# Kernel optimization log

Hardware: AMD Instinct MI355X
Metric: run time of the kernel (lower is better)

The kernel has to match this reference:

```python
import jax, jax.numpy as jnp
import numpy as np

QLEN, MLEN, BSZ, DMODEL, NHEAD, DHEAD = 512, 512, 8, 1024, 16, 64
KLEN = QLEN + MLEN
LN_EPS = 1e-5


def layer_norm(x, g, b):
    mu = jnp.mean(x, axis=-1, keepdims=True)
    var = jnp.var(x, axis=-1, keepdims=True)
    return (x - mu) / jnp.sqrt(var + LN_EPS) * g + b


def rel_shift(x):
    # x: [qlen, klen, bsz, n_head] -- Transformer-XL relative shift trick
    q, k, b, n = x.shape
    x_pad = jnp.pad(x, ((0, 0), (1, 0), (0, 0), (0, 0)))  # zero col at front of dim 1
    x_pad = x_pad.reshape(k + 1, q, b, n)
    return x_pad[1:].reshape(q, k, b, n)


def setup_inputs() -> dict:
    key = jax.random.key(0)
    ks = jax.random.split(key, 10)
    w = lambda k, shape: (jax.random.normal(k, shape, jnp.float32) * 0.02)
    return {
        "content": jax.random.normal(ks[0], (QLEN, BSZ, DMODEL), jnp.float32),
        "mems": jax.random.normal(ks[1], (MLEN, BSZ, DMODEL), jnp.float32),
        "r": jax.random.normal(ks[2], (KLEN, DMODEL), jnp.float32),
        "q_bias": w(ks[3], (NHEAD, DHEAD)),
        "mask": jnp.zeros((QLEN, KLEN, BSZ), jnp.bool_),
        "W_q": w(ks[4], (NHEAD * DHEAD, DMODEL)),
        "W_kv": w(ks[5], (2 * NHEAD * DHEAD, DMODEL)),
        "W_r": w(ks[6], (NHEAD * DHEAD, DMODEL)),
        "b_r": jnp.zeros((NHEAD * DHEAD,), jnp.float32),
        "W_o": w(ks[7], (DMODEL, NHEAD * DHEAD)),
        "b_o": jnp.zeros((DMODEL,), jnp.float32),
        "ln_g": jnp.ones((DMODEL,), jnp.float32),
        "ln_b": jnp.zeros((DMODEL,), jnp.float32),
    }


def reference(content, mems, r, q_bias, mask, W_q, W_kv, W_r, b_r, W_o, b_o, ln_g, ln_b):
    Q, B, D = content.shape
    H, Dh = q_bias.shape
    scale = 1.0 / (Dh ** 0.5)

    c = layer_norm(content, ln_g, ln_b)          # [Q,B,D]
    m = layer_norm(mems, ln_g, ln_b)             # [M,B,D]
    cat = jnp.concatenate([m, c], axis=0)        # [K,B,D]
    K = cat.shape[0]

    kv = cat @ W_kv.T                            # [K,B,2*H*Dh]
    k, v = jnp.split(kv, 2, axis=-1)
    k = k.reshape(K, B, H, Dh)
    v = v.reshape(K, B, H, Dh)

    q = (c @ W_q.T).reshape(Q, B, H, Dh) + q_bias  # [Q,B,H,Dh]
    rproj = (r @ W_r.T + b_r).reshape(K, H, Dh)    # [K,H,Dh]

    AC = jnp.einsum('ibnd,jbnd->ijbn', q, k)       # content-content
    BD = rel_shift(jnp.einsum('ibnd,jnd->ijbn', q, rproj))  # content-position
    score = (AC + BD) * scale                      # [Q,K,B,H]
    score = jnp.where(mask[..., None], -jnp.inf, score)
    prob = jax.nn.softmax(score, axis=1)

    vec = jnp.einsum('ijbn,jbnd->ibnd', prob, v).reshape(Q, B, H * Dh)
    attn_out = vec @ W_o.T + b_o                   # [Q,B,D]
    # IdentityResidualGate: x + relu(y) with x = layer-normed content
    return c + jax.nn.relu(attn_out)
```

## Files before the change

kernel.cpp:

```cpp
#include <hip/hip_runtime.h>
#include <hip/hip_bf16.h>
#include <math.h>

#define QLEN 512
#define MLENC 512
#define KLEN 1024
#define BSZ 8
#define DMODEL 1024
#define NHEAD 16
#define DHEAD 64

typedef __hip_bfloat16 bf16;
typedef unsigned short u16;
typedef unsigned int u32;
typedef __attribute__((ext_vector_type(8))) short s16x8;
typedef __attribute__((ext_vector_type(4))) float f32x4;

#define MFMA16(a, b, c) __builtin_amdgcn_mfma_f32_16x16x32_bf16(a, b, c, 0, 0, 0)

static __device__ __forceinline__ float b2f(bf16 x) { return __bfloat162float(x); }
static __device__ __forceinline__ bf16 f2b(float x) { return __float2bfloat16(x); }
static __device__ __forceinline__ u16 bbu(float x) {
    bf16 h = __float2bfloat16(x);
    return *reinterpret_cast<u16*>(&h);
}
static __device__ __forceinline__ u32 pk2(float a, float b) {
    return ((u32)bbu(b) << 16) | bbu(a);
}

static __device__ __forceinline__ void gl_lds16(const void* g, void* l) {
    __builtin_amdgcn_global_load_lds(
        (const __attribute__((address_space(1))) void*)g,
        (__attribute__((address_space(3))) void*)l, 16, 0, 0);
}

template <int MODE, bool AF32, bool BF32>
static __device__ __forceinline__ void gemm128_dev(const void* __restrict__ Av,
                                                   const void* __restrict__ Bv,
                                                   const float* __restrict__ bias,
                                                   const bf16* __restrict__ resid,
                                                   bf16* __restrict__ Cb,
                                                   float* __restrict__ Cf,
                                                   int m0, int n0, int N,
                                                   short* As, short* Bs) {
    int tid = threadIdx.x;
    int w = tid >> 6, lane = tid & 63, l15 = lane & 15, quad = lane >> 4;
    int wm = w & 1, wn = w >> 1;

    const short* Ab = (const short*)Av;
    const float* Af = (const float*)Av;
    const short* Bb = (const short*)Bv;
    const float* Bf = (const float*)Bv;

    f32x4 acc[4][4];
#pragma unroll
    for (int i = 0; i < 4; ++i)
#pragma unroll
        for (int j = 0; j < 4; ++j) acc[i][j] = (f32x4){0.f, 0.f, 0.f, 0.f};

    for (int kt = 0; kt < 1024; kt += 64) {
        __syncthreads();
        if (!AF32) {
#pragma unroll
            for (int li = 0; li < 4; ++li) {
                int id = (li * 4 + w) * 64 + lane;
                int row = id >> 3;
                int kc = ((id & 7) ^ (row & 7)) * 8;
                gl_lds16(Ab + ((size_t)(m0 + row) * 1024 + kt + kc),
                         &As[(li * 4 + w) * 512]);
            }
        } else {
            int m = tid >> 1, kcl = (tid & 1) * 32;
            const float* src = Af + (size_t)(m0 + m) * 1024 + kt + kcl;
#pragma unroll
            for (int ch = 0; ch < 4; ++ch) {
                int cl = (kcl >> 3) + ch;
                u32* dst = (u32*)&As[m * 64 + ((cl ^ (m & 7)) * 8)];
                float4 f0 = *(const float4*)(src + ch * 8);
                float4 f1 = *(const float4*)(src + ch * 8 + 4);
                dst[0] = pk2(f0.x, f0.y); dst[1] = pk2(f0.z, f0.w);
                dst[2] = pk2(f1.x, f1.y); dst[3] = pk2(f1.z, f1.w);
            }
        }
        if (!BF32) {
#pragma unroll
            for (int li = 0; li < 4; ++li) {
                int id = (li * 4 + w) * 64 + lane;
                int row = id >> 3;
                int kc = ((id & 7) ^ (row & 7)) * 8;
                gl_lds16(Bb + ((size_t)(n0 + row) * 1024 + kt + kc),
                         &Bs[(li * 4 + w) * 512]);
            }
        } else {
            int nn = tid >> 1, kcl = (tid & 1) * 32;
            const float* src = Bf + (size_t)(n0 + nn) * 1024 + kt + kcl;
#pragma unroll
            for (int ch = 0; ch < 4; ++ch) {
                int cl = (kcl >> 3) + ch;
                u32* dst = (u32*)&Bs[nn * 64 + ((cl ^ (nn & 7)) * 8)];
                float4 f0 = *(const float4*)(src + ch * 8);
                float4 f1 = *(const float4*)(src + ch * 8 + 4);
                dst[0] = pk2(f0.x, f0.y); dst[1] = pk2(f0.z, f0.w);
                dst[2] = pk2(f1.x, f1.y); dst[3] = pk2(f1.z, f1.w);
            }
        }
        __syncthreads();

        s16x8 af[4][2], bfr[4][2];
#pragma unroll
        for (int mb = 0; mb < 4; ++mb) {
            int row = wm * 64 + mb * 16 + l15;
#pragma unroll
            for (int kh = 0; kh < 2; ++kh)
                af[mb][kh] = *(const s16x8*)
                    &As[row * 64 + (((kh * 4 + quad) ^ (row & 7)) * 8)];
        }
#pragma unroll
        for (int nb = 0; nb < 4; ++nb) {
            int row = wn * 64 + nb * 16 + l15;
#pragma unroll
            for (int kh = 0; kh < 2; ++kh)
                bfr[nb][kh] = *(const s16x8*)
                    &Bs[row * 64 + (((kh * 4 + quad) ^ (row & 7)) * 8)];
        }
#pragma unroll
        for (int mb = 0; mb < 4; ++mb)
#pragma unroll
            for (int nb = 0; nb < 4; ++nb) {
                acc[mb][nb] = MFMA16(af[mb][0], bfr[nb][0], acc[mb][nb]);
                acc[mb][nb] = MFMA16(af[mb][1], bfr[nb][1], acc[mb][nb]);
            }
    }

#pragma unroll
    for (int mb = 0; mb < 4; ++mb) {
#pragma unroll
        for (int nb = 0; nb < 4; ++nb) {
#pragma unroll
            for (int r = 0; r < 4; ++r) {
                int m = m0 + wm * 64 + mb * 16 + quad * 4 + r;
                int col = n0 + wn * 64 + nb * 16 + l15;
                float v = acc[mb][nb][r];
                if (MODE >= 1) v += bias[col];
                if (MODE == 2) {
                    float rv = b2f(resid[(size_t)m * N + col]);
                    Cf[(size_t)m * N + col] = rv + fmaxf(v, 0.f);
                } else {
                    Cb[(size_t)m * N + col] = f2b(v);
                }
            }
        }
    }
}

template <int MODE, bool AF32, bool BF32>
static __device__ __forceinline__ void gemm64_dev(const void* __restrict__ Av,
                                                  const void* __restrict__ Bv,
                                                  const float* __restrict__ bias,
                                                  const bf16* __restrict__ resid,
                                                  bf16* __restrict__ Cb,
                                                  float* __restrict__ Cf,
                                                  int m0, int n0, int N,
                                                  short* As, short* Bs) {
    int tid = threadIdx.x;
    int w = tid >> 6, lane = tid & 63, l15 = lane & 15, quad = lane >> 4;

    const short* Ab = (const short*)Av;
    const float* Af = (const float*)Av;
    const short* Bb = (const short*)Bv;
    const float* Bf = (const float*)Bv;

    f32x4 acc[4][2];
#pragma unroll
    for (int i = 0; i < 4; ++i)
#pragma unroll
        for (int j = 0; j < 2; ++j) acc[i][j] = (f32x4){0.f, 0.f, 0.f, 0.f};

    for (int kt = 0; kt < 1024; kt += 64) {
        __syncthreads();
        if (!AF32) {
#pragma unroll
            for (int li = 0; li < 2; ++li) {
                int id = (li * 4 + w) * 64 + lane;
                int row = id >> 3;
                int kc = ((id & 7) ^ (row & 7)) * 8;
                gl_lds16(Ab + ((size_t)(m0 + row) * 1024 + kt + kc),
                         &As[(li * 4 + w) * 512]);
            }
        } else {
            int m = tid >> 2, kcl = (tid & 3) * 16;
            const float* src = Af + (size_t)(m0 + m) * 1024 + kt + kcl;
#pragma unroll
            for (int ch = 0; ch < 2; ++ch) {
                int cl = (kcl >> 3) + ch;
                u32* dst = (u32*)&As[m * 64 + ((cl ^ (m & 7)) * 8)];
                float4 f0 = *(const float4*)(src + ch * 8);
                float4 f1 = *(const float4*)(src + ch * 8 + 4);
                dst[0] = pk2(f0.x, f0.y); dst[1] = pk2(f0.z, f0.w);
                dst[2] = pk2(f1.x, f1.y); dst[3] = pk2(f1.z, f1.w);
            }
        }
        if (!BF32) {
#pragma unroll
            for (int li = 0; li < 4; ++li) {
                int id = (li * 4 + w) * 64 + lane;
                int row = id >> 3;
                int kc = ((id & 7) ^ (row & 7)) * 8;
                gl_lds16(Bb + ((size_t)(n0 + row) * 1024 + kt + kc),
                         &Bs[(li * 4 + w) * 512]);
            }
        } else {
            int nn = tid >> 1, kcl = (tid & 1) * 32;
            const float* src = Bf + (size_t)(n0 + nn) * 1024 + kt + kcl;
#pragma unroll
            for (int ch = 0; ch < 4; ++ch) {
                int cl = (kcl >> 3) + ch;
                u32* dst = (u32*)&Bs[nn * 64 + ((cl ^ (nn & 7)) * 8)];
                float4 f0 = *(const float4*)(src + ch * 8);
                float4 f1 = *(const float4*)(src + ch * 8 + 4);
                dst[0] = pk2(f0.x, f0.y); dst[1] = pk2(f0.z, f0.w);
                dst[2] = pk2(f1.x, f1.y); dst[3] = pk2(f1.z, f1.w);
            }
        }
        __syncthreads();

        s16x8 af[4][2], bfr[2][2];
#pragma unroll
        for (int mb = 0; mb < 4; ++mb) {
            int row = mb * 16 + l15;
#pragma unroll
            for (int kh = 0; kh < 2; ++kh)
                af[mb][kh] = *(const s16x8*)
                    &As[row * 64 + (((kh * 4 + quad) ^ (row & 7)) * 8)];
        }
#pragma unroll
        for (int nb = 0; nb < 2; ++nb) {
            int row = w * 32 + nb * 16 + l15;
#pragma unroll
            for (int kh = 0; kh < 2; ++kh)
                bfr[nb][kh] = *(const s16x8*)
                    &Bs[row * 64 + (((kh * 4 + quad) ^ (row & 7)) * 8)];
        }
#pragma unroll
        for (int mb = 0; mb < 4; ++mb)
#pragma unroll
            for (int nb = 0; nb < 2; ++nb) {
                acc[mb][nb] = MFMA16(af[mb][0], bfr[nb][0], acc[mb][nb]);
                acc[mb][nb] = MFMA16(af[mb][1], bfr[nb][1], acc[mb][nb]);
            }
    }

#pragma unroll
    for (int mb = 0; mb < 4; ++mb) {
#pragma unroll
        for (int nb = 0; nb < 2; ++nb) {
#pragma unroll
            for (int r = 0; r < 4; ++r) {
                int m = m0 + mb * 16 + quad * 4 + r;
                int col = n0 + w * 32 + nb * 16 + l15;
                float v = acc[mb][nb][r];
                if (MODE >= 1) v += bias[col];
                if (MODE == 2) {
                    float rv = b2f(resid[(size_t)m * N + col]);
                    Cf[(size_t)m * N + col] = rv + fmaxf(v, 0.f);
                } else {
                    Cb[(size_t)m * N + col] = f2b(v);
                }
            }
        }
    }
}

static __device__ __forceinline__ void ln_body(int row, int tid,
                                               const float* __restrict__ content,
                                               const float* __restrict__ mems,
                                               const float* __restrict__ g,
                                               const float* __restrict__ bet,
                                               bf16* __restrict__ cat,
                                               float* red) {
    const float* src = (row < MLENC * BSZ)
        ? mems + (size_t)row * DMODEL
        : content + (size_t)(row - MLENC * BSZ) * DMODEL;

    float x[4];
    float s = 0.f, ss = 0.f;
#pragma unroll
    for (int l = 0; l < 4; ++l) {
        int d = l * 256 + tid;
        x[l] = src[d];
        s += x[l];
        ss += x[l] * x[l];
    }
#pragma unroll
    for (int off = 32; off > 0; off >>= 1) {
        s  += __shfl_xor(s, off);
        ss += __shfl_xor(ss, off);
    }
    int wid = tid >> 6;
    if ((tid & 63) == 0) { red[wid * 2] = s; red[wid * 2 + 1] = ss; }
    __syncthreads();
    s  = red[0] + red[2] + red[4] + red[6];
    ss = red[1] + red[3] + red[5] + red[7];
    float mu  = s * (1.f / DMODEL);
    float var = ss * (1.f / DMODEL) - mu * mu;
    float rs  = rsqrtf(var + 1e-5f);
    bf16* dst = cat + (size_t)row * DMODEL;
#pragma unroll
    for (int l = 0; l < 4; ++l) {
        int d = l * 256 + tid;
        dst[d] = f2b((x[l] - mu) * rs * g[d] + bet[d]);
    }
}

__global__ __launch_bounds__(256) void ln_kernel(const float* __restrict__ content,
                                                 const float* __restrict__ mems,
                                                 const float* __restrict__ g,
                                                 const float* __restrict__ bet,
                                                 bf16* __restrict__ cat) {
    __shared__ float red[8];
    ln_body(blockIdx.x, threadIdx.x, content, mems, g, bet, cat, red);
}

__global__ __launch_bounds__(256) void prep_kernel(const float* __restrict__ content,
                                                   const float* __restrict__ mems,
                                                   const float* __restrict__ g,
                                                   const float* __restrict__ bet,
                                                   bf16* __restrict__ cat,
                                                   const float* __restrict__ wq,
                                                   const float* __restrict__ wkv,
                                                   const float* __restrict__ wr,
                                                   const float* __restrict__ wo,
                                                   bf16* __restrict__ wout) {
    __shared__ float red[8];
    int bid = blockIdx.x;
    if (bid < KLEN * BSZ) {
        ln_body(bid, threadIdx.x, content, mems, g, bet, cat, red);
    } else {
        int off = ((bid - KLEN * BSZ) * 256 + threadIdx.x) * 8;
        const float* src;
        if (off < 1048576)       src = wq + off;
        else if (off < 3145728)  src = wkv + (off - 1048576);
        else if (off < 4194304)  src = wr + (off - 3145728);
        else                     src = wo + (off - 4194304);
        float4 f0 = *(const float4*)src;
        float4 f1 = *(const float4*)(src + 4);
        s16x8 v;
        v[0] = (short)bbu(f0.x); v[1] = (short)bbu(f0.y);
        v[2] = (short)bbu(f0.z); v[3] = (short)bbu(f0.w);
        v[4] = (short)bbu(f1.x); v[5] = (short)bbu(f1.y);
        v[6] = (short)bbu(f1.z); v[7] = (short)bbu(f1.w);
        *(s16x8*)((short*)wout + off) = v;
    }
}

template <int MODE, bool AF32, bool BF32>
__global__ __launch_bounds__(256) void gemm_mfma(const void* __restrict__ Av,
                                                 const void* __restrict__ Bv,
                                                 const float* __restrict__ bias,
                                                 const bf16* __restrict__ resid,
                                                 bf16* __restrict__ Cb,
                                                 float* __restrict__ Cf,
                                                 int Mr, int N) {
    __shared__ short As[128 * 64];
    __shared__ short Bs[128 * 64];
    gemm128_dev<MODE, AF32, BF32>(Av, Bv, bias, resid, Cb, Cf,
                                  blockIdx.y * 128, blockIdx.x * 128, N, As, Bs);
}

template <int MODE, bool AF32, bool BF32>
__global__ __launch_bounds__(256) void gemm64(const void* __restrict__ Av,
                                              const void* __restrict__ Bv,
                                              const float* __restrict__ bias,
                                              const bf16* __restrict__ resid,
                                              bf16* __restrict__ Cb,
                                              float* __restrict__ Cf,
                                              int Mr, int N) {
    __shared__ short As[64 * 64];
    __shared__ short Bs[128 * 64];
    gemm64_dev<MODE, AF32, BF32>(Av, Bv, bias, resid, Cb, Cf,
                                 blockIdx.y * 64, blockIdx.x * 128, N, As, Bs);
}

__global__ __launch_bounds__(256) void gemms_fused(const bf16* __restrict__ cat,
                                                   const bf16* __restrict__ catc,
                                                   const float* __restrict__ rin,
                                                   const bf16* __restrict__ Wkvb,
                                                   const bf16* __restrict__ Wqb,
                                                   const bf16* __restrict__ Wrb,
                                                   const float* __restrict__ q_bias,
                                                   const float* __restrict__ b_r,
                                                   bf16* __restrict__ kvout,
                                                   bf16* __restrict__ qbout,
                                                   bf16* __restrict__ rpout) {
    __shared__ short As[128 * 64];
    __shared__ short Bs[128 * 64];
    int id = blockIdx.x;
    if (id < 1024) {
        gemm128_dev<0, false, false>(cat, Wkvb, nullptr, nullptr, kvout, nullptr,
                                     (id >> 4) * 128, (id & 15) * 128, 2048, As, Bs);
    } else if (id < 1536) {
        int q = id - 1024;
        gemm64_dev<1, false, false>(catc, Wqb, q_bias, nullptr, qbout, nullptr,
                                    (q >> 3) * 64, (q & 7) * 128, 1024, As, Bs);
    } else {
        int q = id - 1536;
        gemm64_dev<1, true, false>(rin, Wrb, b_r, nullptr, rpout, nullptr,
                                   (q >> 3) * 64, (q & 7) * 128, 1024, As, Bs);
    }
}

__global__ __launch_bounds__(256, 2) void attn_mfma(const bf16* __restrict__ qb,
                                                    const bf16* __restrict__ kv,
                                                    const bf16* __restrict__ rp,
                                                    bf16* __restrict__ vec) {
    __shared__ u16 Ks[64][72];
    __shared__ u16 Vr[2][4096];
    __shared__ u16 Vt[64][72];
    __shared__ u16 Ps[4][16][76];
    __shared__ float Ms[4][16][84];

    int bid = blockIdx.x;
    int it = bid & 7, n = (bid >> 3) & 15, b = bid >> 7;
    int i0 = it * 64;
    int tid = threadIdx.x;
    int w = tid >> 6, lane = tid & 63, l15 = lane & 15, quad = lane >> 4;

    const short* qs = (const short*)qb;
    const short* kvs = (const short*)kv;
    const short* rs = (const short*)rp;

    size_t qoff = (((size_t)(i0 + w * 16 + l15) * 8) + b) * 1024 + n * 64 + quad * 8;
    s16x8 aq0 = *(const s16x8*)(qs + qoff);
    s16x8 aq1 = *(const s16x8*)(qs + qoff + 32);
    int qrow1 = i0 + w * 16 + l15 + 1; if (qrow1 > 511) qrow1 = 511;
    size_t qoffs = (((size_t)qrow1 * 8) + b) * 1024 + n * 64 + quad * 8;
    s16x8 as0 = *(const s16x8*)(qs + qoffs);
    s16x8 as1 = *(const s16x8*)(qs + qoffs + 32);

    f32x4 O0 = {0.f,0.f,0.f,0.f}, O1 = O0, O2 = O0, O3 = O0;
    f32x4 Lacc = O0;
    float mrun[4];
#pragma unroll
    for (int r = 0; r < 4; ++r) mrun[r] = -INFINITY;

    f32x4 z = (f32x4){0.f, 0.f, 0.f, 0.f};
    int ibase = i0 + w * 16 + quad * 4;

    s16x8 ones;
#pragma unroll
    for (int i = 0; i < 8; ++i) ones[i] = (short)0x3F80;

    int r0K = tid >> 3, c0K = (tid & 7) * 8;
    int dV = lane, jV = w * 16;
    int wrow = (3 - w) * 16 + l15;

    auto loadW = [&](int ubase, s16x8* dst) {
#pragma unroll
        for (int ntl = 0; ntl < 5; ++ntl) {
            int u = ubase + wrow + ntl * 16;
            u = u < 0 ? 0 : (u > 1023 ? 1023 : u);
            const short* p = rs + (size_t)u * 1024 + n * 64 + quad * 8;
            dst[ntl * 2]     = *(const s16x8*)p;
            dst[ntl * 2 + 1] = *(const s16x8*)(p + 32);
        }
    };
    auto bandM = [&](const s16x8* wf, s16x8 a0, s16x8 a1, f32x4* th) {
        f32x4 m[5];
#pragma unroll
        for (int ntl = 0; ntl < 5; ++ntl) {
            m[ntl] = MFMA16(a0, wf[ntl * 2], z);
            m[ntl] = MFMA16(a1, wf[ntl * 2 + 1], m[ntl]);
        }
#pragma unroll
        for (int ntl = 0; ntl < 5; ++ntl)
#pragma unroll
            for (int r = 0; r < 4; ++r)
                Ms[w][quad * 4 + r][ntl * 16 + l15] = m[ntl][r];
#pragma unroll
        for (int r = 0; r < 4; ++r) {
            int lr = quad * 4 + r;
            int cb = l15 - lr + 15;
#pragma unroll
            for (int h = 0; h < 4; ++h)
                th[h][r] = Ms[w][lr][cb + 16 * h];
        }
    };

    bool need1c, need2c;
    auto step = [&](int st, s16x8* wcur, s16x8* wnxt) {
        int p = st & 1;
        int j0 = st * 64;
        int d0 = j0 - i0;
        int j0n = (j0 + 64) & 1023;

        __syncthreads();

        size_t base0 = ((size_t)((j0n + r0K) * 8 + b)) * 2048 + n * 64 + c0K;
        size_t base1 = ((size_t)((j0n + 32 + r0K) * 8 + b)) * 2048 + n * 64 + c0K;
        s16x8 kr0 = *(const s16x8*)(kvs + base0);
        s16x8 kr1 = *(const s16x8*)(kvs + base1);
        gl_lds16(kvs + base0 + 1024, &Vr[1 - p][w * 512]);
        gl_lds16(kvs + base1 + 1024, &Vr[1 - p][2048 + w * 512]);

        int d0p = d0 + 64;
        bool need1n = (d0p <= 512);
        bool need2n = (d0p >= 512);
        loadW(need1n ? (448 + d0p) : (d0p - 577), wnxt);

        {
            s16x8 vv0, vv1;
#pragma unroll
            for (int q2 = 0; q2 < 8; ++q2) vv0[q2] = (short)Vr[p][(jV + q2) * 64 + dV];
#pragma unroll
            for (int q2 = 0; q2 < 8; ++q2) vv1[q2] = (short)Vr[p][(jV + 8 + q2) * 64 + dV];
            *(s16x8*)&Vt[dV][jV] = vv0;
            *(s16x8*)&Vt[dV][jV + 8] = vv1;
        }

        f32x4 sc[4];
#pragma unroll
        for (int h = 0; h < 4; ++h) {
            s16x8 bk0 = *(const s16x8*)&Ks[h * 16 + l15][quad * 8];
            s16x8 bk1 = *(const s16x8*)&Ks[h * 16 + l15][32 + quad * 8];
            sc[h] = MFMA16(aq0, bk0, z);
            sc[h] = MFMA16(aq1, bk1, sc[h]);
        }

        f32x4 th1[4], th2[4];
#pragma unroll
        for (int h = 0; h < 4; ++h) { th1[h] = z; th2[h] = z; }
        if (need1c) bandM(wcur, aq0, aq1, th1);
        if (need2c) {
            if (need1c) {
                s16x8 w2[10];
                loadW(d0 - 577, w2);
                bandM(w2, as0, as1, th2);
            } else {
                bandM(wcur, as0, as1, th2);
            }
        }

#pragma unroll
        for (int r = 0; r < 4; ++r) {
            int rr = w * 16 + quad * 4 + r;
            int djb = j0 + l15 - i0 - rr;
#pragma unroll
            for (int h = 0; h < 4; ++h) {
                int dj = djb + 16 * h;
                float bd = (dj <= 512) ? th1[h][r] : ((dj == 513) ? 0.f : th2[h][r]);
                sc[h][r] = (sc[h][r] + bd) * 0.125f;
            }
        }

#pragma unroll
        for (int r = 0; r < 4; ++r) {
            float ml = fmaxf(fmaxf(sc[0][r], sc[1][r]), fmaxf(sc[2][r], sc[3][r]));
            ml = fmaxf(ml, __shfl_xor(ml, 1));
            ml = fmaxf(ml, __shfl_xor(ml, 2));
            ml = fmaxf(ml, __shfl_xor(ml, 4));
            ml = fmaxf(ml, __shfl_xor(ml, 8));
            float mn = fmaxf(mrun[r], ml);
            float p0 = __expf(sc[0][r] - mn);
            float p1 = __expf(sc[1][r] - mn);
            float p2 = __expf(sc[2][r] - mn);
            float p3 = __expf(sc[3][r] - mn);
            float al = __expf(mrun[r] - mn);
            mrun[r] = mn;
            Lacc[r] *= al;
            O0[r] *= al; O1[r] *= al; O2[r] *= al; O3[r] *= al;
            int lr = quad * 4 + r;
            Ps[w][lr][l15]      = bbu(p0);
            Ps[w][lr][16 + l15] = bbu(p1);
            Ps[w][lr][32 + l15] = bbu(p2);
            Ps[w][lr][48 + l15] = bbu(p3);
        }

        __syncthreads();

        s16x8 ap0 = *(const s16x8*)&Ps[w][l15][quad * 8];
        s16x8 ap1 = *(const s16x8*)&Ps[w][l15][32 + quad * 8];
        {
            s16x8 bv0 = *(const s16x8*)&Vt[l15][quad * 8];
            s16x8 bv1 = *(const s16x8*)&Vt[l15][32 + quad * 8];
            O0 = MFMA16(ap0, bv0, O0);
            O0 = MFMA16(ap1, bv1, O0);
        }
        {
            s16x8 bv0 = *(const s16x8*)&Vt[16 + l15][quad * 8];
            s16x8 bv1 = *(const s16x8*)&Vt[16 + l15][32 + quad * 8];
            O1 = MFMA16(ap0, bv0, O1);
            O1 = MFMA16(ap1, bv1, O1);
        }
        {
            s16x8 bv0 = *(const s16x8*)&Vt[32 + l15][quad * 8];
            s16x8 bv1 = *(const s16x8*)&Vt[32 + l15][32 + quad * 8];
            O2 = MFMA16(ap0, bv0, O2);
            O2 = MFMA16(ap1, bv1, O2);
        }
        {
            s16x8 bv0 = *(const s16x8*)&Vt[48 + l15][quad * 8];
            s16x8 bv1 = *(const s16x8*)&Vt[48 + l15][32 + quad * 8];
            O3 = MFMA16(ap0, bv0, O3);
            O3 = MFMA16(ap1, bv1, O3);
        }
        Lacc = MFMA16(ap0, ones, Lacc);
        Lacc = MFMA16(ap1, ones, Lacc);

        *(s16x8*)&Ks[r0K][c0K] = kr0;
        *(s16x8*)&Ks[32 + r0K][c0K] = kr1;
        need1c = need1n;
        need2c = need2n;
    };

    s16x8 wA[10], wB[10];
    {
        size_t base0 = ((size_t)(r0K * 8 + b)) * 2048 + n * 64 + c0K;
        size_t base1 = ((size_t)((32 + r0K) * 8 + b)) * 2048 + n * 64 + c0K;
        s16x8 k0 = *(const s16x8*)(kvs + base0);
        s16x8 k1 = *(const s16x8*)(kvs + base1);
        gl_lds16(kvs + base0 + 1024, &Vr[0][w * 512]);
        gl_lds16(kvs + base1 + 1024, &Vr[0][2048 + w * 512]);
        *(s16x8*)&Ks[r0K][c0K] = k0;
        *(s16x8*)&Ks[32 + r0K][c0K] = k1;
        loadW(448 - i0, wA);
        need1c = true;
        need2c = (-i0 >= 512);
    }

    for (int st2 = 0; st2 < 16; st2 += 2) {
        step(st2,     wA, wB);
        step(st2 + 1, wB, wA);
    }

#pragma unroll
    for (int r = 0; r < 4; ++r) {
        float inv = 1.f / Lacc[r];
        int ig = ibase + r;
        size_t o = ((size_t)ig * 8 + b) * 1024 + n * 64;
        vec[o + l15]      = f2b(O0[r] * inv);
        vec[o + 16 + l15] = f2b(O1[r] * inv);
        vec[o + 32 + l15] = f2b(O2[r] * inv);
        vec[o + 48 + l15] = f2b(O3[r] * inv);
    }
}

extern "C" void kernel_launch(void* const* d_in, const int* in_sizes, int n_in,
                              void* d_out, int out_size, void* d_ws, size_t ws_size,
                              hipStream_t stream) {
    const float* content = (const float*)d_in[0];
    const float* mems    = (const float*)d_in[1];
    const float* r       = (const float*)d_in[2];
    const float* q_bias  = (const float*)d_in[3];
    const float* W_q     = (const float*)d_in[5];
    const float* W_kv    = (const float*)d_in[6];
    const float* W_r     = (const float*)d_in[7];
    const float* b_r     = (const float*)d_in[8];
    const float* W_o     = (const float*)d_in[9];
    const float* b_o     = (const float*)d_in[10];
    const float* ln_g    = (const float*)d_in[11];
    const float* ln_b    = (const float*)d_in[12];

    bf16* ws   = (bf16*)d_ws;
    bf16* cat  = ws;
    bf16* kv   = cat + 8388608;
    bf16* qb   = kv + 16777216;
    bf16* rp   = qb + 4194304;
    bf16* vecb = rp + 1048576;
    bf16* Wb   = vecb + 4194304;
    bf16* catc = cat + (size_t)MLENC * BSZ * DMODEL;

    bf16* Wqb  = Wb;
    bf16* Wkvb = Wb + 1048576;
    bf16* Wrb  = Wb + 3145728;
    bf16* Wob  = Wb + 4194304;

    const size_t FULLW_BYTES = (size_t)(34603008 + 5242880) * 2;
    bool fullw = ws_size >= FULLW_BYTES;

    if (fullw) {
        prep_kernel<<<KLEN * BSZ + 2560, 256, 0, stream>>>(
            content, mems, ln_g, ln_b, cat, W_q, W_kv, W_r, W_o, Wb);

        gemms_fused<<<1664, 256, 0, stream>>>(
            cat, catc, r, Wkvb, Wqb, Wrb, q_bias, b_r, kv, qb, rp);
    } else {
        ln_kernel<<<KLEN * BSZ, 256, 0, stream>>>(content, mems, ln_g, ln_b, cat);
        gemm_mfma<0, false, true><<<dim3(16, 64), 256, 0, stream>>>(
            cat, W_kv, nullptr, nullptr, kv, nullptr, 8192, 2048);
        gemm64<1, false, true><<<dim3(8, 64), 256, 0, stream>>>(
            catc, W_q, q_bias, nullptr, qb, nullptr, 4096, 1024);
        gemm64<1, true, true><<<dim3(8, 16), 256, 0, stream>>>(
            r, W_r, b_r, nullptr, rp, nullptr, 1024, 1024);
    }

    attn_mfma<<<BSZ * NHEAD * 8, 256, 0, stream>>>(qb, kv, rp, vecb);

    if (fullw) {
        gemm64<2, false, false><<<dim3(8, 64), 256, 0, stream>>>(
            vecb, Wob, b_o, catc, nullptr, (float*)d_out, 4096, 1024);
    } else {
        gemm64<2, false, true><<<dim3(8, 64), 256, 0, stream>>>(
            vecb, W_o, b_o, catc, nullptr, (float*)d_out, 4096, 1024);
    }
}
```

Before: 331.3 us.

## Double-buffer K and transposed V tiles to drop a per-step barrier

The attention loop now double-buffers the K tile and the transposed V tile in LDS. V raw loads are prefetched two steps ahead, so the second __syncthreads per KV step can be removed. The band-matrix scratch used for the relative shift is stored as bf16 instead of float, halving its LDS footprint and traffic. This costs extra LDS for the duplicated buffers, a prologue that primes the pipeline, and slight precision loss on the positional scores.

```diff
diff --git a/kernel.cpp b/kernel.cpp
--- a/kernel.cpp
+++ b/kernel.cpp
@@ -23,6 +23,9 @@
 static __device__ __forceinline__ u16 bbu(float x) {
     bf16 h = __float2bfloat16(x);
     return *reinterpret_cast<u16*>(&h);
+}
+static __device__ __forceinline__ float sh2f(u16 v) {
+    return __uint_as_float(((u32)v) << 16);
 }
 static __device__ __forceinline__ u32 pk2(float a, float b) {
     return ((u32)bbu(b) << 16) | bbu(a);
@@ -413,11 +416,11 @@
                                                     const bf16* __restrict__ kv,
                                                     const bf16* __restrict__ rp,
                                                     bf16* __restrict__ vec) {
-    __shared__ u16 Ks[64][72];
+    __shared__ u16 Ks[2][64][72];
     __shared__ u16 Vr[2][4096];
-    __shared__ u16 Vt[64][72];
+    __shared__ u16 Vt[2][64][72];
     __shared__ u16 Ps[4][16][76];
-    __shared__ float Ms[4][16][84];
+    __shared__ u16 Ms[4][16][84];
 
     int bid = blockIdx.x;
     int it = bid & 7, n = (bid >> 3) & 15, b = bid >> 7;
@@ -475,32 +478,38 @@
         for (int ntl = 0; ntl < 5; ++ntl)
 #pragma unroll
             for (int r = 0; r < 4; ++r)
-                Ms[w][quad * 4 + r][ntl * 16 + l15] = m[ntl][r];
+                Ms[w][quad * 4 + r][ntl * 16 + l15] = bbu(m[ntl][r]);
 #pragma unroll
         for (int r = 0; r < 4; ++r) {
             int lr = quad * 4 + r;
             int cb = l15 - lr + 15;
 #pragma unroll
             for (int h = 0; h < 4; ++h)
-                th[h][r] = Ms[w][lr][cb + 16 * h];
+                th[h][r] = sh2f(Ms[w][lr][cb + 16 * h]);
         }
     };
 
     bool need1c, need2c;
     auto step = [&](int st, s16x8* wcur, s16x8* wnxt) {
-        int p = st & 1;
+        int pk = st & 1;
         int j0 = st * 64;
         int d0 = j0 - i0;
-        int j0n = (j0 + 64) & 1023;
+        int j0K = (j0 + 64) & 1023;
+        int j0V = (j0 + 128) & 1023;
 
         __syncthreads();
 
-        size_t base0 = ((size_t)((j0n + r0K) * 8 + b)) * 2048 + n * 64 + c0K;
-        size_t base1 = ((size_t)((j0n + 32 + r0K) * 8 + b)) * 2048 + n * 64 + c0K;
-        s16x8 kr0 = *(const s16x8*)(kvs + base0);
-        s16x8 kr1 = *(const s16x8*)(kvs + base1);
-        gl_lds16(kvs + base0 + 1024, &Vr[1 - p][w * 512]);
-        gl_lds16(kvs + base1 + 1024, &Vr[1 - p][2048 + w * 512]);
+        {
+            size_t vb0 = ((size_t)((j0V + r0K) * 8 + b)) * 2048 + 1024 + n * 64 + c0K;
+            size_t vb1 = ((size_t)((j0V + 32 + r0K) * 8 + b)) * 2048 + 1024 + n * 64 + c0K;
+            gl_lds16(kvs + vb0, &Vr[pk][w * 512]);
+            gl_lds16(kvs + vb1, &Vr[pk][2048 + w * 512]);
+        }
+
+        size_t kb0 = ((size_t)((j0K + r0K) * 8 + b)) * 2048 + n * 64 + c0K;
+        size_t kb1 = ((size_t)((j0K + 32 + r0K) * 8 + b)) * 2048 + n * 64 + c0K;
+        s16x8 kr0 = *(const s16x8*)(kvs + kb0);
+        s16x8 kr1 = *(const s16x8*)(kvs + kb1);
 
         int d0p = d0 + 64;
         bool need1n = (d0p <= 512);
@@ -510,18 +519,18 @@
         {
             s16x8 vv0, vv1;
 #pragma unroll
-            for (int q2 = 0; q2 < 8; ++q2) vv0[q2] = (short)Vr[p][(jV + q2) * 64 + dV];
-#pragma unroll
-            for (int q2 = 0; q2 < 8; ++q2) vv1[q2] = (short)Vr[p][(jV + 8 + q2) * 64 + dV];
-            *(s16x8*)&Vt[dV][jV] = vv0;
-            *(s16x8*)&Vt[dV][jV + 8] = vv1;
+            for (int q2 = 0; q2 < 8; ++q2) vv0[q2] = (short)Vr[1 - pk][(jV + q2) * 64 + dV];
+#pragma unroll
+            for (int q2 = 0; q2 < 8; ++q2) vv1[q2] = (short)Vr[1 - pk][(jV + 8 + q2) * 64 + dV];
+            *(s16x8*)&Vt[1 - pk][dV][jV] = vv0;
+            *(s16x8*)&Vt[1 - pk][dV][jV + 8] = vv1;
         }
 
         f32x4 sc[4];
 #pragma unroll
         for (int h = 0; h < 4; ++h) {
-            s16x8 bk0 = *(const s16x8*)&Ks[h * 16 + l15][quad * 8];
-            s16x8 bk1 = *(const s16x8*)&Ks[h * 16 + l15][32 + quad * 8];
+            s16x8 bk0 = *(const s16x8*)&Ks[pk][h * 16 + l15][quad * 8];
+            s16x8 bk1 = *(const s16x8*)&Ks[pk][h * 16 + l15][32 + quad * 8];
             sc[h] = MFMA16(aq0, bk0, z);
             sc[h] = MFMA16(aq1, bk1, sc[h]);
         }
@@ -575,56 +584,71 @@
             Ps[w][lr][48 + l15] = bbu(p3);
         }
 
-        __syncthreads();
 
         s16x8 ap0 = *(const s16x8*)&Ps[w][l15][quad * 8];
         s16x8 ap1 = *(const s16x8*)&Ps[w][l15][32 + quad * 8];
         {
-            s16x8 bv0 = *(const s16x8*)&Vt[l15][quad * 8];
-            s16x8 bv1 = *(const s16x8*)&Vt[l15][32 + quad * 8];
+            s16x8 bv0 = *(const s16x8*)&Vt[pk][l15][quad * 8];
+            s16x8 bv1 = *(const s16x8*)&Vt[pk][l15][32 + quad * 8];
             O0 = MFMA16(ap0, bv0, O0);
             O0 = MFMA16(ap1, bv1, O0);
         }
         {
-            s16x8 bv0 = *(const s16x8*)&Vt[16 + l15][quad * 8];
-            s16x8 bv1 = *(const s16x8*)&Vt[16 + l15][32 + quad * 8];
+            s16x8 bv0 = *(const s16x8*)&Vt[pk][16 + l15][quad * 8];
+            s16x8 bv1 = *(const s16x8*)&Vt[pk][16 + l15][32 + quad * 8];
             O1 = MFMA16(ap0, bv0, O1);
             O1 = MFMA16(ap1, bv1, O1);
         }
         {
-            s16x8 bv0 = *(const s16x8*)&Vt[32 + l15][quad * 8];
-            s16x8 bv1 = *(const s16x8*)&Vt[32 + l15][32 + quad * 8];
+            s16x8 bv0 = *(const s16x8*)&Vt[pk][32 + l15][quad * 8];
+            s16x8 bv1 = *(const s16x8*)&Vt[pk][32 + l15][32 + quad * 8];
             O2 = MFMA16(ap0, bv0, O2);
             O2 = MFMA16(ap1, bv1, O2);
         }
         {
-            s16x8 bv0 = *(const s16x8*)&Vt[48 + l15][quad * 8];
-            s16x8 bv1 = *(const s16x8*)&Vt[48 + l15][32 + quad * 8];
+            s16x8 bv0 = *(const s16x8*)&Vt[pk][48 + l15][quad * 8];
+            s16x8 bv1 = *(const s16x8*)&Vt[pk][48 + l15][32 + quad * 8];
             O3 = MFMA16(ap0, bv0, O3);
             O3 = MFMA16(ap1, bv1, O3);
         }
         Lacc = MFMA16(ap0, ones, Lacc);
         Lacc = MFMA16(ap1, ones, Lacc);
 
-        *(s16x8*)&Ks[r0K][c0K] = kr0;
-        *(s16x8*)&Ks[32 + r0K][c0K] = kr1;
+        *(s16x8*)&Ks[1 - pk][r0K][c0K] = kr0;
+        *(s16x8*)&Ks[1 - pk][32 + r0K][c0K] = kr1;
         need1c = need1n;
         need2c = need2n;
     };
 
     s16x8 wA[10], wB[10];
     {
-        size_t base0 = ((size_t)(r0K * 8 + b)) * 2048 + n * 64 + c0K;
-        size_t base1 = ((size_t)((32 + r0K) * 8 + b)) * 2048 + n * 64 + c0K;
-        s16x8 k0 = *(const s16x8*)(kvs + base0);
-        s16x8 k1 = *(const s16x8*)(kvs + base1);
-        gl_lds16(kvs + base0 + 1024, &Vr[0][w * 512]);
-        gl_lds16(kvs + base1 + 1024, &Vr[0][2048 + w * 512]);
-        *(s16x8*)&Ks[r0K][c0K] = k0;
-        *(s16x8*)&Ks[32 + r0K][c0K] = k1;
+        size_t kb0 = ((size_t)(r0K * 8 + b)) * 2048 + n * 64 + c0K;
+        size_t kb1 = ((size_t)((32 + r0K) * 8 + b)) * 2048 + n * 64 + c0K;
+        s16x8 k0 = *(const s16x8*)(kvs + kb0);
+        s16x8 k1 = *(const s16x8*)(kvs + kb1);
+        gl_lds16(kvs + kb0 + 1024, &Vr[0][w * 512]);
+        gl_lds16(kvs + kb1 + 1024, &Vr[0][2048 + w * 512]);
+        *(s16x8*)&Ks[0][r0K][c0K] = k0;
+        *(s16x8*)&Ks[0][32 + r0K][c0K] = k1;
         loadW(448 - i0, wA);
         need1c = true;
-        need2c = (-i0 >= 512);
+        need2c = false;
+    }
+    __syncthreads();
+    {
+        s16x8 vv0, vv1;
+#pragma unroll
+        for (int q2 = 0; q2 < 8; ++q2) vv0[q2] = (short)Vr[0][(jV + q2) * 64 + dV];
+#pragma unroll
+        for (int q2 = 0; q2 < 8; ++q2) vv1[q2] = (short)Vr[0][(jV + 8 + q2) * 64 + dV];
+        *(s16x8*)&Vt[0][dV][jV] = vv0;
+        *(s16x8*)&Vt[0][dV][jV + 8] = vv1;
+    }
+    {
+        size_t vb0 = ((size_t)((64 + r0K) * 8 + b)) * 2048 + 1024 + n * 64 + c0K;
+        size_t vb1 = ((size_t)((96 + r0K) * 8 + b)) * 2048 + 1024 + n * 64 + c0K;
+        gl_lds16(kvs + vb0, &Vr[1][w * 512]);
+        gl_lds16(kvs + vb1, &Vr[1][2048 + w * 512]);
     }
 
     for (int st2 = 0; st2 < 16; st2 += 2) {
```

Result: no change. 332.9 us (+0.5%).
